# Optimization experiments

Measured on AMD Instinct MI355X. Metric: run time of the kernel, lower is better.

The kernel has to match this reference:

```python
import jax, jax.numpy as jnp
import numpy as np

R1, R2, KHOPS = 8, 4, 2


def topk_adj(S, k):
    # top-k neighbors per row (self excluded), symmetrized 0/1 adjacency
    n = S.shape[-1]
    S = jnp.where(jnp.eye(n, dtype=bool), -jnp.inf, S)
    _, idx = jax.lax.top_k(S, k)  # [..., n, k]
    rows = jnp.arange(n)[:, None]

    def one(ix):
        return jnp.zeros((n, n), jnp.float32).at[rows, ix].set(1.0)

    A = jax.vmap(one)(idx.reshape(-1, n, k)).reshape(S.shape)
    return jnp.maximum(A, jnp.swapaxes(A, -1, -2))


def gcn_norm(A):
    # GCNConv normalization with self-loops: D^-1/2 (A+I) D^-1/2
    Ah = A + jnp.eye(A.shape[-1], dtype=A.dtype)
    dinv = jax.lax.rsqrt(Ah.sum(-1))
    return Ah * dinv[..., :, None] * dinv[..., None, :]


def khop_reach(A, k):
    # boolean reachability within k hops (k_hop_subgraph node sets), incl. self
    n = A.shape[-1]
    R = jnp.broadcast_to(jnp.eye(n, dtype=bool), A.shape)
    for _ in range(k):
        R = R | (jnp.einsum('...ij,...jk->...ik', R.astype(A.dtype), A) > 0)
    return R


def sub_gcn_pool(A, R, Y, bias):
    # per-center-node subgraph GCNConv + global_max_pool, batched over centers
    # A:[n,n] adjacency, R:[n,n] bool subgraph membership, Y:[n,f] = X @ W
    Rf = R.astype(Y.dtype)
    deg = 1.0 + jnp.einsum('jk,ik->ij', A, Rf)  # [center i, node j]: in-subgraph degree + self-loop
    dinv = jnp.where(R, jax.lax.rsqrt(deg), 0.0)
    T = jnp.einsum('jk,ikf->ijf', A, dinv[:, :, None] * Y[None])  # neighbor aggregation inside subgraph i
    Z = dinv[:, :, None] * T + (dinv ** 2)[:, :, None] * Y[None] + bias
    Z = jnp.where(R[:, :, None], Z, -jnp.inf)
    return Z.max(axis=1)  # global_max_pool per subgraph -> [n, f]


def _forward(x, pe_inter, pe_dim, W_time, b_time, W_sub, b_sub, W_dim, b_dim,
             c1w, c1b, c2w, c2b, dm1w, dm1b, dm2w, dm2b):
    B, D, N, L = x.shape
    # ---- stage 1: per-dimension temporal graphs (inter_topk) + per-dim GCNConv
    S = jnp.einsum('bdnl,bdml->bdnm', x, x)
    A_t = topk_adj(S, R1)  # [B,D,N,N]
    feat = jnp.concatenate([x, jnp.broadcast_to(pe_inter, (B, D) + pe_inter.shape)], axis=-1)
    h = jnp.einsum('bdnm,bdmf->bdnf', gcn_norm(A_t),
                   jnp.einsum('bdnl,dlf->bdnf', feat, W_time)) + b_time[None, :, None, :]
    # ---- stage 2: inter-dimension graph per batch element (intra_topk)
    feat2 = jnp.concatenate([h.reshape(B, D, -1), jnp.broadcast_to(pe_dim, (B,) + pe_dim.shape)], axis=-1)
    S2 = jnp.einsum('bdf,bef->bde', feat2, feat2)
    A_d = topk_adj(S2, R2)  # [B,D,D]
    # ---- stage 3: k-hop subgraph GCN + per-subgraph max pool
    R = khop_reach(A_d, KHOPS)
    Y = jnp.einsum('bdf,fg->bdg', feat2, W_sub)
    pooled = jax.vmap(sub_gcn_pool, in_axes=(0, 0, 0, None))(A_d, R, Y, b_sub)  # [B,D,d2]
    # ---- stage 4: dim-level GCN on the full dim graph
    dim_out = jnp.einsum('bde,beg->bdg', gcn_norm(A_d),
                         jnp.einsum('bdg,gh->bdh', pooled, W_dim)) + b_dim  # [B,D,d2]
    # ---- heads (ReverseLayerF is identity in the forward pass)
    dom = jax.nn.relu(dim_out.reshape(B * D, -1) @ dm1w + dm1b) @ dm2w + dm2b  # [B*D, D]
    g_pool = dim_out.max(axis=1)  # global_max_pool over dim -> [B, d2]
    task = jax.nn.relu(g_pool @ c1w + c1b) @ c2w + c2b  # [B, num_class]
    return task, dom, g_pool


def setup_inputs() -> dict:
    key = jax.random.key(0)
    ks = jax.random.split(key, 10)
    B, D, N, L = 16, 64, 128, 256
    d1, d2, NC = 64, 128, 2
    pe1, pe2 = N // 4, D // 4
    s = lambda f: 1.0 / float(np.sqrt(f))
    return dict(
        x=jax.random.normal(ks[0], (B, D, N, L), jnp.float32),
        pe_inter=jax.random.normal(ks[1], (N, pe1), jnp.float32) * 0.02,
        pe_dim=jax.random.normal(ks[2], (D, pe2), jnp.float32) * 0.02,
        W_time=jax.random.normal(ks[3], (D, L + pe1, d1), jnp.float32) * s(L + pe1),
        b_time=jnp.zeros((D, d1), jnp.float32),
        W_sub=jax.random.normal(ks[4], (N * d1 + pe2, d2), jnp.float32) * s(N * d1 + pe2),
        b_sub=jnp.zeros((d2,), jnp.float32),
        W_dim=jax.random.normal(ks[5], (d2, d2), jnp.float32) * s(d2),
        b_dim=jnp.zeros((d2,), jnp.float32),
        c1w=jax.random.normal(ks[6], (d2, d2), jnp.float32) * s(d2),
        c1b=jnp.zeros((d2,), jnp.float32),
        c2w=jax.random.normal(ks[7], (d2, NC), jnp.float32) * s(d2),
        c2b=jnp.zeros((NC,), jnp.float32),
        dm1w=jax.random.normal(ks[8], (d2, d2), jnp.float32) * s(d2),
        dm1b=jnp.zeros((d2,), jnp.float32),
        dm2w=jax.random.normal(ks[9], (d2, D), jnp.float32) * s(d2),
        dm2b=jnp.zeros((D,), jnp.float32),
    )


def reference(x, pe_inter, pe_dim, W_time, b_time, W_sub, b_sub, W_dim, b_dim,
              c1w, c1b, c2w, c2b, dm1w, dm1b, dm2w, dm2b):
    return _forward(x, pe_inter, pe_dim, W_time, b_time, W_sub, b_sub, W_dim, b_dim,
                    c1w, c1b, c2w, c2b, dm1w, dm1b, dm2w, dm2b)
```

## Files before the change

### kernel.cpp

```cpp
#include <hip/hip_runtime.h>
#include <stdint.h>

namespace {
constexpr int B_ = 16, D_ = 64, N_ = 128, L_ = 256;
constexpr int PE1 = 32, F1 = L_ + PE1;
constexpr int D1 = 64;
constexpr int ND1 = N_ * D1;
constexpr int PE2 = 16, F2 = ND1 + PE2;
constexpr int D2 = 128;
constexpr int NC_ = 2;
constexpr int TOPK1 = 8, TOPK2 = 4;
constexpr int NP = B_ * D_;
constexpr int KS2 = 32, S2CH = 257;
constexpr int KSY = 32, YCH = 257;
}

__device__ __forceinline__ int ctz32(unsigned int m) { return __builtin_ctz(m); }
__device__ __forceinline__ int ctz64(uint64_t m) { return __builtin_ctzll(m); }
__device__ __forceinline__ int pop64(uint64_t m) { return __builtin_popcountll(m); }

__global__ __launch_bounds__(256) void k_S_topk(const float* __restrict__ x,
                                                uint32_t* __restrict__ bits1,
                                                float* __restrict__ dinv1) {
  int p = blockIdx.x;
  const float* X = x + (size_t)p * N_ * L_;
  __shared__ float Xt[32 * 132];
  __shared__ unsigned int bits[N_][4];
  int t = threadIdx.x, tx = t & 15, ty = t >> 4;
  for (int i = t; i < N_ * 4; i += 256) ((unsigned int*)bits)[i] = 0u;
  float acc[8][8] = {};
  for (int k0 = 0; k0 < L_; k0 += 32) {
    __syncthreads();
    for (int i = t; i < N_ * 32; i += 256) {
      int kk = i & 31, n = i >> 5;
      Xt[kk * 132 + n] = X[n * L_ + k0 + kk];
    }
    __syncthreads();
    for (int kk = 0; kk < 32; ++kk) {
      float a[8], bb[8];
      #pragma unroll
      for (int r = 0; r < 8; ++r) a[r] = Xt[kk * 132 + ty * 8 + r];
      #pragma unroll
      for (int c = 0; c < 8; ++c) bb[c] = Xt[kk * 132 + tx * 8 + c];
      #pragma unroll
      for (int r = 0; r < 8; ++r)
        #pragma unroll
        for (int c = 0; c < 8; ++c) acc[r][c] += a[r] * bb[c];
    }
  }
  if (tx == ty) {
    #pragma unroll
    for (int r = 0; r < 8; ++r) acc[r][r] = -INFINITY;
  }
  #pragma unroll
  for (int r = 0; r < 8; ++r) {
    int row = ty * 8 + r;
    for (int it = 0; it < TOPK1; ++it) {
      float bv = acc[r][0]; int bc = 0;
      #pragma unroll
      for (int c = 1; c < 8; ++c)
        if (acc[r][c] > bv) { bv = acc[r][c]; bc = c; }
      int bidx = tx * 8 + bc;
      #pragma unroll
      for (int off = 1; off < 16; off <<= 1) {
        float ov = __shfl_xor(bv, off);
        int   oi = __shfl_xor(bidx, off);
        if (ov > bv || (ov == bv && oi < bidx)) { bv = ov; bidx = oi; }
      }
      #pragma unroll
      for (int c = 0; c < 8; ++c)
        if (tx * 8 + c == bidx) acc[r][c] = -INFINITY;
      if (tx == 0) {
        atomicOr(&bits[row][bidx >> 5], 1u << (bidx & 31));
        atomicOr(&bits[bidx][row >> 5], 1u << (row & 31));
      }
    }
  }
  __syncthreads();
  if (t < N_) {
    int deg = 1;
    for (int w = 0; w < 4; ++w) deg += __popc(bits[t][w]);
    dinv1[(size_t)p * N_ + t] = rsqrtf((float)deg);
  }
  for (int i = t; i < N_ * 4; i += 256)
    bits1[(size_t)p * 512 + i] = ((unsigned int*)bits)[i];
}

__global__ __launch_bounds__(256) void k_G(const float* __restrict__ x,
                                           const float* __restrict__ pe_inter,
                                           const float* __restrict__ W_time,
                                           const float* __restrict__ dinv1,
                                           float* __restrict__ G) {
  int p = blockIdx.x, d = p & 63;
  const float* X = x + (size_t)p * N_ * L_;
  const float* W = W_time + (size_t)d * F1 * D1;
  __shared__ float Ft[32 * 132];
  __shared__ float Wt[32 * 64];
  __shared__ float dvs[N_];
  int t = threadIdx.x, tx = t & 15, ty = t >> 4;
  if (t < N_) dvs[t] = dinv1[(size_t)p * N_ + t];
  float acc[8][4] = {};
  for (int k0 = 0; k0 < F1; k0 += 32) {
    __syncthreads();
    for (int i = t; i < N_ * 32; i += 256) {
      int kk = i & 31, n = i >> 5, k = k0 + kk;
      Ft[kk * 132 + n] = (k < L_) ? X[n * L_ + k] : pe_inter[n * PE1 + (k - L_)];
    }
    for (int i = t; i < 32 * D1; i += 256) {
      int f = i & 63, kk = i >> 6;
      Wt[kk * 64 + f] = W[(k0 + kk) * D1 + f];
    }
    __syncthreads();
    for (int kk = 0; kk < 32; ++kk) {
      float a[8], bb[4];
      #pragma unroll
      for (int r = 0; r < 8; ++r) a[r] = Ft[kk * 132 + ty * 8 + r];
      #pragma unroll
      for (int c = 0; c < 4; ++c) bb[c] = Wt[kk * 64 + tx * 4 + c];
      #pragma unroll
      for (int r = 0; r < 8; ++r)
        #pragma unroll
        for (int c = 0; c < 4; ++c) acc[r][c] += a[r] * bb[c];
    }
  }
  float* Gp = G + (size_t)p * N_ * D1;
  for (int r = 0; r < 8; ++r) {
    float dv = dvs[ty * 8 + r];
    #pragma unroll
    for (int c = 0; c < 4; ++c)
      Gp[(ty * 8 + r) * D1 + tx * 4 + c] = acc[r][c] * dv;
  }
}

__global__ __launch_bounds__(256) void k_h(const float* __restrict__ G,
                                           const uint32_t* __restrict__ bits1,
                                           const float* __restrict__ dinv1,
                                           const float* __restrict__ b_time,
                                           float* __restrict__ h) {
  int p = blockIdx.x, d = p & 63;
  __shared__ float Gs[N_ * D1];
  __shared__ unsigned int bs[N_][4];
  __shared__ float dvs[N_];
  int t = threadIdx.x;
  if (t < N_) dvs[t] = dinv1[(size_t)p * N_ + t];
  for (int i = t; i < N_ * 4; i += 256)
    ((unsigned int*)bs)[i] = bits1[(size_t)p * 512 + i];
  for (int i = t; i < N_ * D1; i += 256) Gs[i] = G[(size_t)p * N_ * D1 + i];
  __syncthreads();
  int f = t & 63, wg = t >> 6;
  const float* bt = b_time + d * D1;
  float* hp = h + (size_t)p * N_ * D1;
  for (int row = wg; row < N_; row += 4) {
    float a = Gs[row * D1 + f];
    #pragma unroll
    for (int w = 0; w < 4; ++w) {
      unsigned int m = bs[row][w];
      while (m) { int j = (w << 5) + ctz32(m); m &= m - 1; a += Gs[j * D1 + f]; }
    }
    hp[row * D1 + f] = dvs[row] * a + bt[f];
  }
}

__global__ __launch_bounds__(256) void k_S2p(const float* __restrict__ h,
                                             const float* __restrict__ pe_dim,
                                             float* __restrict__ S2p) {
  int b = blockIdx.x, s = blockIdx.y;
  int k0 = s * S2CH, kend = k0 + S2CH; if (kend > F2) kend = F2;
  __shared__ float Ft[D_][33];
  int t = threadIdx.x, tx = t & 15, ty = t >> 4;
  float acc[4][4] = {};
  for (int kt = k0; kt < kend; kt += 32) {
    for (int i = t; i < D_ * 32; i += 256) {
      int kk = i & 31, dd = i >> 5, k = kt + kk;
      float v = 0.f;
      if (k < kend)
        v = (k < ND1) ? h[(((size_t)b * D_ + dd) * N_ + (k >> 6)) * D1 + (k & 63)]
                      : pe_dim[dd * PE2 + (k - ND1)];
      Ft[dd][kk] = v;
    }
    __syncthreads();
    for (int kk = 0; kk < 32; ++kk) {
      float a[4], bb[4];
      #pragma unroll
      for (int r = 0; r < 4; ++r) a[r] = Ft[ty * 4 + r][kk];
      #pragma unroll
      for (int c = 0; c < 4; ++c) bb[c] = Ft[tx * 4 + c][kk];
      #pragma unroll
      for (int r = 0; r < 4; ++r)
        #pragma unroll
        for (int c = 0; c < 4; ++c) acc[r][c] += a[r] * bb[c];
    }
    __syncthreads();
  }
  float* out = S2p + (size_t)(b * KS2 + s) * D_ * D_;
  for (int r = 0; r < 4; ++r)
    for (int c = 0; c < 4; ++c)
      out[(ty * 4 + r) * D_ + tx * 4 + c] = acc[r][c];
}

__global__ __launch_bounds__(256) void k_dimgraph(const float* __restrict__ S2p,
                                                  uint64_t* __restrict__ Adb,
                                                  uint64_t* __restrict__ Rb,
                                                  float* __restrict__ dinvA) {
  int b = blockIdx.x;
  __shared__ float S2s[D_][D_ + 1];
  __shared__ unsigned int bits[D_][2];
  __shared__ uint64_t Ads[D_];
  int t = threadIdx.x, lane = t & 63, wave = t >> 6;
  for (int i = t; i < D_ * D_; i += 256) {
    float acc = 0.f;
    for (int s = 0; s < KS2; ++s) acc += S2p[(size_t)(b * KS2 + s) * D_ * D_ + i];
    S2s[i >> 6][i & 63] = acc;
  }
  if (t < D_ * 2) ((unsigned int*)bits)[t] = 0u;
  __syncthreads();
  for (int r = wave; r < D_; r += 4) {
    float v = S2s[r][lane];
    if (lane == r) v = -INFINITY;
    for (int it = 0; it < TOPK2; ++it) {
      float bv = v; int idx = lane;
      for (int off = 32; off; off >>= 1) {
        float ov = __shfl_xor(bv, off);
        int   oi = __shfl_xor(idx, off);
        if (ov > bv || (ov == bv && oi < idx)) { bv = ov; idx = oi; }
      }
      if (idx == lane) v = -INFINITY;
      if (lane == 0) {
        atomicOr(&bits[r][idx >> 5], 1u << (idx & 31));
        atomicOr(&bits[idx][r >> 5], 1u << (r & 31));
      }
    }
  }
  __syncthreads();
  if (t < D_) {
    uint64_t m = ((uint64_t)bits[t][1] << 32) | (uint64_t)bits[t][0];
    Ads[t] = m;
    Adb[b * D_ + t] = m;
    dinvA[b * D_ + t] = rsqrtf((float)(pop64(m) + 1));
  }
  __syncthreads();
  if (t < D_) {
    uint64_t r1 = Ads[t] | (1ull << t);
    uint64_t r2 = r1, m = r1;
    while (m) { int j = ctz64(m); m &= m - 1; r2 |= Ads[j]; }
    Rb[b * D_ + t] = r2;
  }
}

__global__ __launch_bounds__(256) void k_Yp(const float* __restrict__ h,
                                            const float* __restrict__ pe_dim,
                                            const float* __restrict__ W_sub,
                                            float* __restrict__ Yp) {
  int b = blockIdx.x, s = blockIdx.y;
  int k0 = s * YCH, kend = k0 + YCH; if (kend > F2) kend = F2;
  __shared__ float Ft[D_][33];
  __shared__ float Wt[32][D2];
  int t = threadIdx.x, tx = t & 15, ty = t >> 4;
  float acc[4][8] = {};
  for (int kt = k0; kt < kend; kt += 32) {
    for (int i = t; i < D_ * 32; i += 256) {
      int kk = i & 31, dd = i >> 5, k = kt + kk;
      float v = 0.f;
      if (k < kend)
        v = (k < ND1) ? h[(((size_t)b * D_ + dd) * N_ + (k >> 6)) * D1 + (k & 63)]
                      : pe_dim[dd * PE2 + (k - ND1)];
      Ft[dd][kk] = v;
    }
    for (int i = t; i < 32 * D2; i += 256) {
      int g = i & 127, kk = i >> 7, k = kt + kk;
      Wt[kk][g] = (k < kend) ? W_sub[(size_t)k * D2 + g] : 0.f;
    }
    __syncthreads();
    for (int kk = 0; kk < 32; ++kk) {
      float a[4], bb[8];
      #pragma unroll
      for (int r = 0; r < 4; ++r) a[r] = Ft[ty * 4 + r][kk];
      #pragma unroll
      for (int c = 0; c < 8; ++c) bb[c] = Wt[kk][tx * 8 + c];
      #pragma unroll
      for (int r = 0; r < 4; ++r)
        #pragma unroll
        for (int c = 0; c < 8; ++c) acc[r][c] += a[r] * bb[c];
    }
    __syncthreads();
  }
  float* out = Yp + (size_t)(b * KSY + s) * D_ * D2;
  for (int r = 0; r < 4; ++r)
    for (int c = 0; c < 8; ++c)
      out[(ty * 4 + r) * D2 + tx * 8 + c] = acc[r][c];
}

__global__ __launch_bounds__(256) void k_Yred(const float* __restrict__ Yp,
                                              float* __restrict__ Y) {
  int i = blockIdx.x * 256 + threadIdx.x;
  int b = i >> 13, r = i & 8191;
  float acc = 0.f;
  for (int s = 0; s < KSY; ++s) acc += Yp[(size_t)(b * KSY + s) * 8192 + r];
  Y[i] = acc;
}

__global__ __launch_bounds__(128) void k_pool(const float* __restrict__ Y,
                                              const uint64_t* __restrict__ Adb,
                                              const uint64_t* __restrict__ Rb,
                                              const float* __restrict__ b_sub,
                                              float* __restrict__ pooled) {
  int blk = blockIdx.x, b = blk >> 6, i = blk & 63;
  __shared__ float Ys[D_][D2];
  __shared__ float dv[D_];
  __shared__ uint64_t Ads[D_];
  int t = threadIdx.x;
  uint64_t Ri = Rb[b * D_ + i];
  for (int idx = t; idx < D_ * D2; idx += 128)
    Ys[idx >> 7][idx & 127] = Y[(size_t)b * D_ * D2 + idx];
  if (t < D_) {
    uint64_t aj = Adb[b * D_ + t];
    Ads[t] = aj;
    dv[t] = ((Ri >> t) & 1) ? rsqrtf((float)(1 + pop64(aj & Ri))) : 0.f;
  }
  __syncthreads();
  int f = t;
  float best = -INFINITY;
  uint64_t mj = Ri;
  while (mj) {
    int j = ctz64(mj); mj &= mj - 1;
    float T = 0.f;
    uint64_t mk = Ads[j] & Ri;
    while (mk) { int k = ctz64(mk); mk &= mk - 1; T += dv[k] * Ys[k][f]; }
    float dj = dv[j];
    float z = dj * T + dj * dj * Ys[j][f] + b_sub[f];
    best = fmaxf(best, z);
  }
  pooled[((size_t)b * D_ + i) * D2 + f] = best;
}

__global__ __launch_bounds__(256) void k_dim(const float* __restrict__ pooled,
                                             const float* __restrict__ W_dim,
                                             const uint64_t* __restrict__ Adb,
                                             const float* __restrict__ dinvA,
                                             const float* __restrict__ b_dim,
                                             float* __restrict__ dimout) {
  int b = blockIdx.x;
  __shared__ float Ps[D_ * D2];
  __shared__ float dva[D_];
  __shared__ uint64_t Ads[D_];
  int t = threadIdx.x, tx = t & 15, ty = t >> 4;
  if (t < D_) { dva[t] = dinvA[b * D_ + t]; Ads[t] = Adb[b * D_ + t]; }
  for (int i = t; i < D_ * D2; i += 256)
    Ps[i] = pooled[(size_t)b * D_ * D2 + i];
  __syncthreads();
  float acc[4][8] = {};
  for (int k = 0; k < D2; ++k) {
    float a[4], bb[8];
    #pragma unroll
    for (int c = 0; c < 8; ++c) bb[c] = W_dim[k * D2 + tx * 8 + c];
    #pragma unroll
    for (int r = 0; r < 4; ++r) a[r] = Ps[(ty * 4 + r) * D2 + k];
    #pragma unroll
    for (int r = 0; r < 4; ++r)
      #pragma unroll
      for (int c = 0; c < 8; ++c) acc[r][c] += a[r] * bb[c];
  }
  __syncthreads();
  for (int r = 0; r < 4; ++r) {
    float dv = dva[ty * 4 + r];
    #pragma unroll
    for (int c = 0; c < 8; ++c)
      Ps[(ty * 4 + r) * D2 + tx * 8 + c] = acc[r][c] * dv;
  }
  __syncthreads();
  int g = t & 127, rg = t >> 7;
  for (int row = rg; row < D_; row += 2) {
    float a = Ps[row * D2 + g];
    uint64_t m = Ads[row];
    while (m) { int e = ctz64(m); m &= m - 1; a += Ps[e * D2 + g]; }
    dimout[((size_t)b * D_ + row) * D2 + g] = dva[row] * a + b_dim[g];
  }
}

__global__ __launch_bounds__(256) void k_dom(const float* __restrict__ dimout,
                                             const float* __restrict__ dm1w,
                                             const float* __restrict__ dm1b,
                                             const float* __restrict__ dm2w,
                                             const float* __restrict__ dm2b,
                                             float* __restrict__ dom) {
  __shared__ float vrow[4][D2];
  __shared__ float hid[4][D2];
  int t = threadIdx.x, lane = t & 63, wave = t >> 6;
  int row = blockIdx.x * 4 + wave;
  const float* v = dimout + (size_t)row * D2;
  for (int i = lane; i < D2; i += 64) vrow[wave][i] = v[i];
  __syncthreads();
  for (int u = lane; u < D2; u += 64) {
    float a = dm1b[u];
    for (int k = 0; k < D2; ++k) a += vrow[wave][k] * dm1w[k * D2 + u];
    hid[wave][u] = fmaxf(a, 0.f);
  }
  __syncthreads();
  float a = dm2b[lane];
  for (int k = 0; k < D2; ++k) a += hid[wave][k] * dm2w[k * D_ + lane];
  dom[(size_t)row * D_ + lane] = a;
}

__global__ __launch_bounds__(128) void k_task(const float* __restrict__ dimout,
                                              const float* __restrict__ c1w,
                                              const float* __restrict__ c1b,
                                              const float* __restrict__ c2w,
                                              const float* __restrict__ c2b,
                                              float* __restrict__ task,
                                              float* __restrict__ g_pool) {
  int b = blockIdx.x, f = threadIdx.x;
  __shared__ float gp[D2], hid[D2];
  float m = -INFINITY;
  for (int d = 0; d < D_; ++d)
    m = fmaxf(m, dimout[((size_t)b * D_ + d) * D2 + f]);
  gp[f] = m;
  g_pool[b * D2 + f] = m;
  __syncthreads();
  float a = c1b[f];
  for (int k = 0; k < D2; ++k) a += gp[k] * c1w[k * D2 + f];
  hid[f] = fmaxf(a, 0.f);
  __syncthreads();
  if (f < NC_) {
    float o = c2b[f];
    for (int k = 0; k < D2; ++k) o += hid[k] * c2w[k * NC_ + f];
    task[b * NC_ + f] = o;
  }
}

extern "C" void kernel_launch(void* const* d_in, const int* in_sizes, int n_in,
                              void* d_out, int out_size, void* d_ws, size_t ws_size,
                              hipStream_t stream) {
  const float* x        = (const float*)d_in[0];
  const float* pe_inter = (const float*)d_in[1];
  const float* pe_dim   = (const float*)d_in[2];
  const float* W_time   = (const float*)d_in[3];
  const float* b_time   = (const float*)d_in[4];
  const float* W_sub    = (const float*)d_in[5];
  const float* b_sub    = (const float*)d_in[6];
  const float* W_dim    = (const float*)d_in[7];
  const float* b_dim    = (const float*)d_in[8];
  const float* c1w      = (const float*)d_in[9];
  const float* c1b      = (const float*)d_in[10];
  const float* c2w      = (const float*)d_in[11];
  const float* c2b      = (const float*)d_in[12];
  const float* dm1w     = (const float*)d_in[13];
  const float* dm1b     = (const float*)d_in[14];
  const float* dm2w     = (const float*)d_in[15];
  const float* dm2b     = (const float*)d_in[16];

  float* out     = (float*)d_out;
  float* task_o  = out;
  float* dom_o   = out + B_ * NC_;
  float* gpool_o = out + B_ * NC_ + NP * D_;

  char* w = (char*)d_ws;
  size_t o = 0;
  auto alloc = [&](size_t bytes) { void* p = w + o; o += (bytes + 255) & ~(size_t)255; return p; };

  float*    hbuf  = (float*)alloc((size_t)NP * N_ * D1 * 4);
  uint32_t* bits1 = (uint32_t*)alloc((size_t)NP * 512 * 4);
  float*    dinv1 = (float*)alloc((size_t)NP * N_ * 4);
  float*    S2p   = (float*)alloc((size_t)B_ * KS2 * D_ * D_ * 4);
  uint64_t* Adb   = (uint64_t*)alloc((size_t)B_ * D_ * 8);
  uint64_t* Rb    = (uint64_t*)alloc((size_t)B_ * D_ * 8);
  float*    dinvA = (float*)alloc((size_t)B_ * D_ * 4);
  float*    Yp    = (float*)alloc((size_t)B_ * KSY * D_ * D2 * 4);
  float*    Y     = (float*)alloc((size_t)B_ * D_ * D2 * 4);
  float*    pooled= (float*)alloc((size_t)B_ * D_ * D2 * 4);
  float*    dimout= (float*)alloc((size_t)B_ * D_ * D2 * 4);
  (void)ws_size; (void)in_sizes; (void)n_in; (void)out_size;

  float* Gbuf = S2p;

  k_S_topk <<<NP, 256, 0, stream>>>(x, bits1, dinv1);
  k_G      <<<NP, 256, 0, stream>>>(x, pe_inter, W_time, dinv1, Gbuf);
  k_h      <<<NP, 256, 0, stream>>>(Gbuf, bits1, dinv1, b_time, hbuf);
  dim3 g5(B_, KS2);
  k_S2p    <<<g5, 256, 0, stream>>>(hbuf, pe_dim, S2p);
  k_dimgraph<<<B_, 256, 0, stream>>>(S2p, Adb, Rb, dinvA);
  dim3 g8(B_, KSY);
  k_Yp     <<<g8, 256, 0, stream>>>(hbuf, pe_dim, W_sub, Yp);
  k_Yred   <<<(B_ * D_ * D2) / 256, 256, 0, stream>>>(Yp, Y);
  k_pool   <<<B_ * D_, 128, 0, stream>>>(Y, Adb, Rb, b_sub, pooled);
  k_dim    <<<B_, 256, 0, stream>>>(pooled, W_dim, Adb, dinvA, b_dim, dimout);
  k_dom    <<<NP / 4, 256, 0, stream>>>(dimout, dm1w, dm1b, dm2w, dm2b, dom_o);
  k_task   <<<B_, 128, 0, stream>>>(dimout, c1w, c1b, c2w, c2b, task_o, gpool_o);
}
```

Measured before the change: 751.6 us.

## Fuse G projection with neighbor aggregation and widen stage-1 blocks to 512 threads

Merges the k_G and k_h kernels so the dinv-scaled feature projection stays in shared memory and is aggregated over the top-k adjacency bits in the same block. This removes a global write and read of the G intermediate and one launch. Both k_S_topk and the fused kernel now run 512 threads with half the per-thread register tile, aiming for more parallelism per block. The cost is a larger shared-memory footprint for the fused kernel, and the topk kernel needs a rewritten diagonal-masking step.

```diff
diff --git a/kernel.cpp b/kernel.cpp
--- a/kernel.cpp
+++ b/kernel.cpp
@@ -19,42 +19,43 @@
 __device__ __forceinline__ int ctz64(uint64_t m) { return __builtin_ctzll(m); }
 __device__ __forceinline__ int pop64(uint64_t m) { return __builtin_popcountll(m); }
 
-__global__ __launch_bounds__(256) void k_S_topk(const float* __restrict__ x,
-                                                uint32_t* __restrict__ bits1,
-                                                float* __restrict__ dinv1) {
+__global__ __launch_bounds__(512, 8) void k_S_topk(const float* __restrict__ x,
+                                                   uint32_t* __restrict__ bits1,
+                                                   float* __restrict__ dinv1) {
   int p = blockIdx.x;
   const float* X = x + (size_t)p * N_ * L_;
   __shared__ float Xt[32 * 132];
   __shared__ unsigned int bits[N_][4];
   int t = threadIdx.x, tx = t & 15, ty = t >> 4;
-  for (int i = t; i < N_ * 4; i += 256) ((unsigned int*)bits)[i] = 0u;
-  float acc[8][8] = {};
+  if (t < N_ * 4) ((unsigned int*)bits)[t] = 0u;
+  float acc[4][8] = {};
   for (int k0 = 0; k0 < L_; k0 += 32) {
     __syncthreads();
-    for (int i = t; i < N_ * 32; i += 256) {
+    for (int i = t; i < N_ * 32; i += 512) {
       int kk = i & 31, n = i >> 5;
       Xt[kk * 132 + n] = X[n * L_ + k0 + kk];
     }
     __syncthreads();
     for (int kk = 0; kk < 32; ++kk) {
-      float a[8], bb[8];
-      #pragma unroll
-      for (int r = 0; r < 8; ++r) a[r] = Xt[kk * 132 + ty * 8 + r];
+      float a[4], bb[8];
+      #pragma unroll
+      for (int r = 0; r < 4; ++r) a[r] = Xt[kk * 132 + ty * 4 + r];
       #pragma unroll
       for (int c = 0; c < 8; ++c) bb[c] = Xt[kk * 132 + tx * 8 + c];
       #pragma unroll
-      for (int r = 0; r < 8; ++r)
+      for (int r = 0; r < 4; ++r)
         #pragma unroll
         for (int c = 0; c < 8; ++c) acc[r][c] += a[r] * bb[c];
     }
   }
-  if (tx == ty) {
-    #pragma unroll
-    for (int r = 0; r < 8; ++r) acc[r][r] = -INFINITY;
-  }
   #pragma unroll
-  for (int r = 0; r < 8; ++r) {
-    int row = ty * 8 + r;
+  for (int r = 0; r < 4; ++r)
+    #pragma unroll
+    for (int c = 0; c < 8; ++c)
+      if (ty * 4 + r == tx * 8 + c) acc[r][c] = -INFINITY;
+  #pragma unroll
+  for (int r = 0; r < 4; ++r) {
+    int row = ty * 4 + r;
     for (int it = 0; it < TOPK1; ++it) {
       float bv = acc[r][0]; int bc = 0;
       #pragma unroll
@@ -82,80 +83,69 @@
     for (int w = 0; w < 4; ++w) deg += __popc(bits[t][w]);
     dinv1[(size_t)p * N_ + t] = rsqrtf((float)deg);
   }
-  for (int i = t; i < N_ * 4; i += 256)
-    bits1[(size_t)p * 512 + i] = ((unsigned int*)bits)[i];
-}
-
-__global__ __launch_bounds__(256) void k_G(const float* __restrict__ x,
-                                           const float* __restrict__ pe_inter,
-                                           const float* __restrict__ W_time,
-                                           const float* __restrict__ dinv1,
-                                           float* __restrict__ G) {
+  if (t < N_ * 4)
+    bits1[(size_t)p * 512 + t] = ((unsigned int*)bits)[t];
+}
+
+__global__ __launch_bounds__(512, 8) void k_G_h(const float* __restrict__ x,
+                                                const float* __restrict__ pe_inter,
+                                                const float* __restrict__ W_time,
+                                                const uint32_t* __restrict__ bits1,
+                                                const float* __restrict__ dinv1,
+                                                const float* __restrict__ b_time,
+                                                float* __restrict__ h) {
   int p = blockIdx.x, d = p & 63;
   const float* X = x + (size_t)p * N_ * L_;
   const float* W = W_time + (size_t)d * F1 * D1;
-  __shared__ float Ft[32 * 132];
-  __shared__ float Wt[32 * 64];
+  __shared__ float smem[N_ * D1];
+  __shared__ unsigned int bs[N_][4];
   __shared__ float dvs[N_];
+  float* Ft = smem;
+  float* Wt = smem + 4224;
   int t = threadIdx.x, tx = t & 15, ty = t >> 4;
   if (t < N_) dvs[t] = dinv1[(size_t)p * N_ + t];
-  float acc[8][4] = {};
+  if (t < N_ * 4) ((unsigned int*)bs)[t] = bits1[(size_t)p * 512 + t];
+  float acc[4][4] = {};
   for (int k0 = 0; k0 < F1; k0 += 32) {
     __syncthreads();
-    for (int i = t; i < N_ * 32; i += 256) {
+    for (int i = t; i < N_ * 32; i += 512) {
       int kk = i & 31, n = i >> 5, k = k0 + kk;
       Ft[kk * 132 + n] = (k < L_) ? X[n * L_ + k] : pe_inter[n * PE1 + (k - L_)];
     }
-    for (int i = t; i < 32 * D1; i += 256) {
+    for (int i = t; i < 32 * D1; i += 512) {
       int f = i & 63, kk = i >> 6;
       Wt[kk * 64 + f] = W[(k0 + kk) * D1 + f];
     }
     __syncthreads();
     for (int kk = 0; kk < 32; ++kk) {
-      float a[8], bb[4];
-      #pragma unroll
-      for (int r = 0; r < 8; ++r) a[r] = Ft[kk * 132 + ty * 8 + r];
+      float a[4], bb[4];
+      #pragma unroll
+      for (int r = 0; r < 4; ++r) a[r] = Ft[kk * 132 + ty * 4 + r];
       #pragma unroll
       for (int c = 0; c < 4; ++c) bb[c] = Wt[kk * 64 + tx * 4 + c];
       #pragma unroll
-      for (int r = 0; r < 8; ++r)
+      for (int r = 0; r < 4; ++r)
         #pragma unroll
         for (int c = 0; c < 4; ++c) acc[r][c] += a[r] * bb[c];
     }
   }
-  float* Gp = G + (size_t)p * N_ * D1;
-  for (int r = 0; r < 8; ++r) {
-    float dv = dvs[ty * 8 + r];
+  __syncthreads();
+  for (int r = 0; r < 4; ++r) {
+    float dv = dvs[ty * 4 + r];
     #pragma unroll
     for (int c = 0; c < 4; ++c)
-      Gp[(ty * 8 + r) * D1 + tx * 4 + c] = acc[r][c] * dv;
-  }
-}
-
-__global__ __launch_bounds__(256) void k_h(const float* __restrict__ G,
-                                           const uint32_t* __restrict__ bits1,
-                                           const float* __restrict__ dinv1,
-                                           const float* __restrict__ b_time,
-                                           float* __restrict__ h) {
-  int p = blockIdx.x, d = p & 63;
-  __shared__ float Gs[N_ * D1];
-  __shared__ unsigned int bs[N_][4];
-  __shared__ float dvs[N_];
-  int t = threadIdx.x;
-  if (t < N_) dvs[t] = dinv1[(size_t)p * N_ + t];
-  for (int i = t; i < N_ * 4; i += 256)
-    ((unsigned int*)bs)[i] = bits1[(size_t)p * 512 + i];
-  for (int i = t; i < N_ * D1; i += 256) Gs[i] = G[(size_t)p * N_ * D1 + i];
+      smem[(ty * 4 + r) * D1 + tx * 4 + c] = acc[r][c] * dv;
+  }
   __syncthreads();
   int f = t & 63, wg = t >> 6;
   const float* bt = b_time + d * D1;
   float* hp = h + (size_t)p * N_ * D1;
-  for (int row = wg; row < N_; row += 4) {
-    float a = Gs[row * D1 + f];
+  for (int row = wg; row < N_; row += 8) {
+    float a = smem[row * D1 + f];
     #pragma unroll
     for (int w = 0; w < 4; ++w) {
       unsigned int m = bs[row][w];
-      while (m) { int j = (w << 5) + ctz32(m); m &= m - 1; a += Gs[j * D1 + f]; }
+      while (m) { int j = (w << 5) + ctz32(m); m &= m - 1; a += smem[j * D1 + f]; }
     }
     hp[row * D1 + f] = dvs[row] * a + bt[f];
   }
@@ -470,11 +460,8 @@
   float*    dimout= (float*)alloc((size_t)B_ * D_ * D2 * 4);
   (void)ws_size; (void)in_sizes; (void)n_in; (void)out_size;
 
-  float* Gbuf = S2p;
-
-  k_S_topk <<<NP, 256, 0, stream>>>(x, bits1, dinv1);
-  k_G      <<<NP, 256, 0, stream>>>(x, pe_inter, W_time, dinv1, Gbuf);
-  k_h      <<<NP, 256, 0, stream>>>(Gbuf, bits1, dinv1, b_time, hbuf);
+  k_S_topk <<<NP, 512, 0, stream>>>(x, bits1, dinv1);
+  k_G_h    <<<NP, 512, 0, stream>>>(x, pe_inter, W_time, bits1, dinv1, b_time, hbuf);
   dim3 g5(B_, KS2);
   k_S2p    <<<g5, 256, 0, stream>>>(hbuf, pe_dim, S2p);
   k_dimgraph<<<B_, 256, 0, stream>>>(S2p, Adb, Rb, dinvA);
```

Measured after the change: 700.0 us. -6.9%, faster.
